# Performance work log

Hardware: AMD Instinct MI355X
Metric: run time of the kernel (lower is better)

The kernel has to match this reference:

```python
import jax, jax.numpy as jnp
import numpy as np

BASE = 7.0  # ModularPhaseNorm modulus


def _plane_rotate(x, theta):
    # Rotate the first 2*P dims of x in P independent 2D planes by learned angles theta [P].
    P = theta.shape[0]
    c, s = jnp.cos(theta), jnp.sin(theta)  # [P]
    head = x[..., : 2 * P].reshape(x.shape[:-1] + (P, 2))
    a, b = head[..., 0], head[..., 1]
    rot = jnp.stack([c * a - s * b, s * a + c * b], axis=-1)
    rot = rot.reshape(x.shape[:-1] + (2 * P,))
    return jnp.concatenate([rot, x[..., 2 * P :]], axis=-1)


def _modular_phase_norm(x, gamma, beta, base=BASE):
    # Wrap activations into [-base/2, base/2) (modular phase), then affine per-channel.
    wrapped = x - base * jnp.floor(x / base + 0.5)
    return gamma * wrapped + beta


def setup_inputs() -> dict:
    key = jax.random.key(0)
    ks = jax.random.split(key, 8)
    B, F, T, H = 8192, 4096, 9, 32
    team_paths = jax.random.normal(ks[0], (B, F, T), dtype=jnp.float32)
    W1 = jax.random.normal(ks[1], (F, H), dtype=jnp.float32) / np.sqrt(F)
    b1 = jnp.zeros((H,), dtype=jnp.float32)
    theta1 = jax.random.normal(ks[2], (2,), dtype=jnp.float32)  # num_rotation_planes=2
    gamma = jnp.ones((H,), dtype=jnp.float32)
    beta = jnp.zeros((H,), dtype=jnp.float32)
    W2 = jax.random.normal(ks[3], (H, 1), dtype=jnp.float32) / np.sqrt(H)
    b2 = jnp.zeros((1,), dtype=jnp.float32)
    theta2 = jax.random.normal(ks[4], (2,), dtype=jnp.float32)
    return {"team_paths": team_paths, "theta1": theta1, "W1": W1, "b1": b1,
            "gamma": gamma, "beta": beta, "theta2": theta2, "W2": W2, "b2": b2}


def reference(team_paths, theta1, W1, b1, gamma, beta, theta2, W2, b2):
    # Batch the per-member Python loop: [B, F, T] -> [B, T, F]
    x = jnp.transpose(team_paths, (0, 2, 1))
    # eidosTransform(feature_dim -> 32, 2 rotation planes)
    h = _plane_rotate(x, theta1)
    h = jnp.einsum("btf,fh->bth", h, W1) + b1
    # ModularPhaseNorm(32, base=7)
    h = _modular_phase_norm(h, gamma, beta)
    # eidosTransform(32 -> 1, 2 rotation planes)
    h = _plane_rotate(h, theta2)
    scores = jnp.einsum("bth,ho->bto", h, W2)[..., 0] + b2[0]  # [B, T]
    return jax.nn.softmax(scores, axis=1)
```

## Files before the change

kernel.cpp:

```cpp
#include <hip/hip_runtime.h>
#include <math.h>

typedef float f2v __attribute__((ext_vector_type(2)));
typedef float f4v __attribute__((ext_vector_type(4)));

#define NTILE 16
#define TILE_W 2304
#define FT 36864

__global__ __launch_bounds__(256) void scorer_kernel(
    const float* __restrict__ x,
    const float* __restrict__ th1,
    const float* __restrict__ W1,
    const float* __restrict__ b1,
    const float* __restrict__ gamma,
    const float* __restrict__ beta,
    const float* __restrict__ th2,
    const float* __restrict__ W2,
    const float* __restrict__ b2p,
    float* __restrict__ out)
{
    __shared__ __align__(16) float xl[2 * TILE_W];
    const int tid = threadIdx.x;
    const int hg  = tid & 7;
    const int fc  = tid >> 3;
    const int wv  = tid >> 6;
    const float* xb = x + (size_t)blockIdx.x * FT;

    f2v acc[9][2];
    #pragma unroll
    for (int t = 0; t < 9; ++t) {
        acc[t][0] = (f2v){0.f, 0.f};
        acc[t][1] = (f2v){0.f, 0.f};
    }

    int laddr[9];
    #pragma unroll
    for (int j = 0; j < 9; ++j) {
        int w = (j < 4) ? tid * 4 + j
              : (j < 8) ? 1024 + tid * 4 + (j - 4)
                        : 2048 + tid;
        int f = (unsigned)w / 9u;
        int t = w - 9 * f;
        laddr[j] = t * 256 + f;
    }

    f4v s04 = __builtin_nontemporal_load((const f4v*)(xb + tid * 4));
    f4v s47 = __builtin_nontemporal_load((const f4v*)(xb + 1024 + tid * 4));
    float s8 = __builtin_nontemporal_load(xb + 2048 + tid);

    const f4v* __restrict__ W1v = (const f4v*)W1;
    int cur = 0;
    for (int tile = 0; tile < NTILE; ++tile) {
        __syncthreads();
        float* lb = &xl[cur * TILE_W];
        lb[laddr[0]] = s04.x; lb[laddr[1]] = s04.y;
        lb[laddr[2]] = s04.z; lb[laddr[3]] = s04.w;
        lb[laddr[4]] = s47.x; lb[laddr[5]] = s47.y;
        lb[laddr[6]] = s47.z; lb[laddr[7]] = s47.w;
        lb[laddr[8]] = s8;
        __syncthreads();
        if (tile + 1 < NTILE) {
            const float* gt = xb + (size_t)(tile + 1) * TILE_W;
            s04 = __builtin_nontemporal_load((const f4v*)(gt + tid * 4));
            s47 = __builtin_nontemporal_load((const f4v*)(gt + 1024 + tid * 4));
            s8  = __builtin_nontemporal_load(gt + 2048 + tid);
        }
        if (tile == 0) {
            if (tid < 18) {
                int p = tid / 9, t = tid - p * 9;
                float c = cosf(th1[p]), sn = sinf(th1[p]);
                float a  = xl[t * 256 + 2 * p];
                float bv = xl[t * 256 + 2 * p + 1];
                xl[t * 256 + 2 * p]     = c * a - sn * bv;
                xl[t * 256 + 2 * p + 1] = sn * a + c * bv;
            }
            __syncthreads();
        }
        const int fb = tile * 256;
        f2v wlo[8], whi[8];
        #pragma unroll
        for (int i = 0; i < 8; ++i) {
            f4v wq = W1v[(size_t)(fb + fc * 8 + i) * 8 + hg];
            wlo[i] = (f2v){wq.x, wq.y};
            whi[i] = (f2v){wq.z, wq.w};
        }
        const float* xr = &xl[cur * TILE_W + fc * 8];
        #pragma unroll
        for (int t = 0; t < 9; ++t) {
            f4v xa = *(const f4v*)(xr + t * 256);
            f4v xc = *(const f4v*)(xr + t * 256 + 4);
            acc[t][0] += (f2v){xa.x, xa.x} * wlo[0]; acc[t][1] += (f2v){xa.x, xa.x} * whi[0];
            acc[t][0] += (f2v){xa.y, xa.y} * wlo[1]; acc[t][1] += (f2v){xa.y, xa.y} * whi[1];
            acc[t][0] += (f2v){xa.z, xa.z} * wlo[2]; acc[t][1] += (f2v){xa.z, xa.z} * whi[2];
            acc[t][0] += (f2v){xa.w, xa.w} * wlo[3]; acc[t][1] += (f2v){xa.w, xa.w} * whi[3];
            acc[t][0] += (f2v){xc.x, xc.x} * wlo[4]; acc[t][1] += (f2v){xc.x, xc.x} * whi[4];
            acc[t][0] += (f2v){xc.y, xc.y} * wlo[5]; acc[t][1] += (f2v){xc.y, xc.y} * whi[5];
            acc[t][0] += (f2v){xc.z, xc.z} * wlo[6]; acc[t][1] += (f2v){xc.z, xc.z} * whi[6];
            acc[t][0] += (f2v){xc.w, xc.w} * wlo[7]; acc[t][1] += (f2v){xc.w, xc.w} * whi[7];
        }
        cur ^= 1;
    }

    const int lane = tid & 63;
    float* red = xl;
    float* redbase = &red[(wv * 8 + lane) * 36];
    #pragma unroll
    for (int t = 0; t < 9; ++t)
        #pragma unroll
        for (int jv = 0; jv < 2; ++jv) {
            f2v v = acc[t][jv];
            v.x += __shfl_xor(v.x, 8);  v.y += __shfl_xor(v.y, 8);
            v.x += __shfl_xor(v.x, 16); v.y += __shfl_xor(v.y, 16);
            v.x += __shfl_xor(v.x, 32); v.y += __shfl_xor(v.y, 32);
            if (lane < 8) {
                redbase[t * 4 + jv * 2]     = v.x;
                redbase[t * 4 + jv * 2 + 1] = v.y;
            }
        }
    __syncthreads();

    for (int o = tid; o < 288; o += 256) {
        int h = o & 31, t = o >> 5;
        int hg2 = h >> 2, j = h & 3;
        int idx = t * 4 + j;
        float v = red[(0 * 8 + hg2) * 36 + idx]
                + red[(1 * 8 + hg2) * 36 + idx]
                + red[(2 * 8 + hg2) * 36 + idx]
                + red[(3 * 8 + hg2) * 36 + idx];
        v += b1[h];
        float wr = v - 7.0f * floorf(v / 7.0f + 0.5f);
        xl[1200 + o] = gamma[h] * wr + beta[h];
    }
    __syncthreads();

    if (tid < 9) {
        const float* g = &xl[1200 + tid * 32];
        float c0 = cosf(th2[0]), s0 = sinf(th2[0]);
        float c1 = cosf(th2[1]), s1 = sinf(th2[1]);
        float sc = (c0 * g[0] - s0 * g[1]) * W2[0]
                 + (s0 * g[0] + c0 * g[1]) * W2[1]
                 + (c1 * g[2] - s1 * g[3]) * W2[2]
                 + (s1 * g[2] + c1 * g[3]) * W2[3];
        #pragma unroll
        for (int h = 4; h < 32; ++h) sc += g[h] * W2[h];
        sc += b2p[0];
        xl[1500 + tid] = sc;
    }
    __syncthreads();

    if (tid < 9) {
        const float* sb = &xl[1500];
        float m = sb[0];
        #pragma unroll
        for (int k = 1; k < 9; ++k) m = fmaxf(m, sb[k]);
        float den = 0.f;
        #pragma unroll
        for (int k = 0; k < 9; ++k) den += expf(sb[k] - m);
        out[(size_t)blockIdx.x * 9 + tid] = expf(sb[tid] - m) / den;
    }
}

extern "C" void kernel_launch(void* const* d_in, const int* in_sizes, int n_in,
                              void* d_out, int out_size, void* d_ws, size_t ws_size,
                              hipStream_t stream) {
    const float* x     = (const float*)d_in[0];
    const float* th1   = (const float*)d_in[1];
    const float* W1    = (const float*)d_in[2];
    const float* b1    = (const float*)d_in[3];
    const float* gamma = (const float*)d_in[4];
    const float* beta  = (const float*)d_in[5];
    const float* th2   = (const float*)d_in[6];
    const float* W2    = (const float*)d_in[7];
    const float* b2    = (const float*)d_in[8];
    float* out = (float*)d_out;

    const int B = in_sizes[0] / FT;
    dim3 grid(B), block(256);
    hipLaunchKernelGGL(scorer_kernel, grid, block, 0, stream,
                       x, th1, W1, b1, gamma, beta, th2, W2, b2, out);
}
```

Measured before the change: 426.0 us.

## Remap threads to 4 features x 8 hidden units and pad LDS rows

Reassigns each thread from 8 features x 4 hidden outputs to 4 features x 8 hidden outputs, doubling accumulators per thread and halving W1 rows read per thread. LDS rows are padded from 256 to 260 floats to reduce bank conflicts on the per-timestep reads. The cross-lane reduction gains one shuffle stage and the reduction and scratch layouts are reworked to match. Register pressure rises from the larger accumulator array.

```diff
diff --git a/kernel.cpp b/kernel.cpp
--- a/kernel.cpp
+++ b/kernel.cpp
@@ -5,7 +5,8 @@
 typedef float f4v __attribute__((ext_vector_type(4)));
 
 #define NTILE 16
-#define TILE_W 2304
+#define FPAD 260
+#define TILE_PAD (9 * FPAD)
 #define FT 36864
 
 __global__ __launch_bounds__(256) void scorer_kernel(
@@ -20,19 +21,18 @@
     const float* __restrict__ b2p,
     float* __restrict__ out)
 {
-    __shared__ __align__(16) float xl[2 * TILE_W];
+    __shared__ __align__(16) float xl[2 * TILE_PAD];
     const int tid = threadIdx.x;
-    const int hg  = tid & 7;
-    const int fc  = tid >> 3;
+    const int hg  = tid & 3;
+    const int fc  = tid >> 2;
     const int wv  = tid >> 6;
     const float* xb = x + (size_t)blockIdx.x * FT;
 
-    f2v acc[9][2];
+    f2v acc[9][4];
     #pragma unroll
-    for (int t = 0; t < 9; ++t) {
-        acc[t][0] = (f2v){0.f, 0.f};
-        acc[t][1] = (f2v){0.f, 0.f};
-    }
+    for (int t = 0; t < 9; ++t)
+        #pragma unroll
+        for (int q = 0; q < 4; ++q) acc[t][q] = (f2v){0.f, 0.f};
 
     int laddr[9];
     #pragma unroll
@@ -42,7 +42,7 @@
                         : 2048 + tid;
         int f = (unsigned)w / 9u;
         int t = w - 9 * f;
-        laddr[j] = t * 256 + f;
+        laddr[j] = t * FPAD + f;
     }
 
     f4v s04 = __builtin_nontemporal_load((const f4v*)(xb + tid * 4));
@@ -53,7 +53,7 @@
     int cur = 0;
     for (int tile = 0; tile < NTILE; ++tile) {
         __syncthreads();
-        float* lb = &xl[cur * TILE_W];
+        float* lb = &xl[cur * TILE_PAD];
         lb[laddr[0]] = s04.x; lb[laddr[1]] = s04.y;
         lb[laddr[2]] = s04.z; lb[laddr[3]] = s04.w;
         lb[laddr[4]] = s47.x; lb[laddr[5]] = s47.y;
@@ -61,7 +61,7 @@
         lb[laddr[8]] = s8;
         __syncthreads();
         if (tile + 1 < NTILE) {
-            const float* gt = xb + (size_t)(tile + 1) * TILE_W;
+            const float* gt = xb + (size_t)(tile + 1) * 2304;
             s04 = __builtin_nontemporal_load((const f4v*)(gt + tid * 4));
             s47 = __builtin_nontemporal_load((const f4v*)(gt + 1024 + tid * 4));
             s8  = __builtin_nontemporal_load(gt + 2048 + tid);
@@ -70,72 +70,72 @@
             if (tid < 18) {
                 int p = tid / 9, t = tid - p * 9;
                 float c = cosf(th1[p]), sn = sinf(th1[p]);
-                float a  = xl[t * 256 + 2 * p];
-                float bv = xl[t * 256 + 2 * p + 1];
-                xl[t * 256 + 2 * p]     = c * a - sn * bv;
-                xl[t * 256 + 2 * p + 1] = sn * a + c * bv;
+                float a  = xl[t * FPAD + 2 * p];
+                float bv = xl[t * FPAD + 2 * p + 1];
+                xl[t * FPAD + 2 * p]     = c * a - sn * bv;
+                xl[t * FPAD + 2 * p + 1] = sn * a + c * bv;
             }
             __syncthreads();
         }
+        const float* xbuf = &xl[cur * TILE_PAD];
         const int fb = tile * 256;
-        f2v wlo[8], whi[8];
         #pragma unroll
-        for (int i = 0; i < 8; ++i) {
-            f4v wq = W1v[(size_t)(fb + fc * 8 + i) * 8 + hg];
-            wlo[i] = (f2v){wq.x, wq.y};
-            whi[i] = (f2v){wq.z, wq.w};
-        }
-        const float* xr = &xl[cur * TILE_W + fc * 8];
-        #pragma unroll
-        for (int t = 0; t < 9; ++t) {
-            f4v xa = *(const f4v*)(xr + t * 256);
-            f4v xc = *(const f4v*)(xr + t * 256 + 4);
-            acc[t][0] += (f2v){xa.x, xa.x} * wlo[0]; acc[t][1] += (f2v){xa.x, xa.x} * whi[0];
-            acc[t][0] += (f2v){xa.y, xa.y} * wlo[1]; acc[t][1] += (f2v){xa.y, xa.y} * whi[1];
-            acc[t][0] += (f2v){xa.z, xa.z} * wlo[2]; acc[t][1] += (f2v){xa.z, xa.z} * whi[2];
-            acc[t][0] += (f2v){xa.w, xa.w} * wlo[3]; acc[t][1] += (f2v){xa.w, xa.w} * whi[3];
-            acc[t][0] += (f2v){xc.x, xc.x} * wlo[4]; acc[t][1] += (f2v){xc.x, xc.x} * whi[4];
-            acc[t][0] += (f2v){xc.y, xc.y} * wlo[5]; acc[t][1] += (f2v){xc.y, xc.y} * whi[5];
-            acc[t][0] += (f2v){xc.z, xc.z} * wlo[6]; acc[t][1] += (f2v){xc.z, xc.z} * whi[6];
-            acc[t][0] += (f2v){xc.w, xc.w} * wlo[7]; acc[t][1] += (f2v){xc.w, xc.w} * whi[7];
+        for (int ih = 0; ih < 2; ++ih) {
+            const int f0 = fb + fc * 4 + ih * 2;
+            f4v wa0 = W1v[(size_t)f0 * 8 + hg * 2];
+            f4v wa1 = W1v[(size_t)f0 * 8 + hg * 2 + 1];
+            f4v wb0 = W1v[(size_t)(f0 + 1) * 8 + hg * 2];
+            f4v wb1 = W1v[(size_t)(f0 + 1) * 8 + hg * 2 + 1];
+            const float* xr = xbuf + fc * 4 + ih * 2;
+            #pragma unroll
+            for (int t = 0; t < 9; ++t) {
+                f2v xp = *(const f2v*)(xr + t * FPAD);
+                f2v xa = {xp.x, xp.x}, xc = {xp.y, xp.y};
+                acc[t][0] += xa * (f2v){wa0.x, wa0.y};
+                acc[t][1] += xa * (f2v){wa0.z, wa0.w};
+                acc[t][2] += xa * (f2v){wa1.x, wa1.y};
+                acc[t][3] += xa * (f2v){wa1.z, wa1.w};
+                acc[t][0] += xc * (f2v){wb0.x, wb0.y};
+                acc[t][1] += xc * (f2v){wb0.z, wb0.w};
+                acc[t][2] += xc * (f2v){wb1.x, wb1.y};
+                acc[t][3] += xc * (f2v){wb1.z, wb1.w};
+            }
         }
         cur ^= 1;
     }
 
     const int lane = tid & 63;
     float* red = xl;
-    float* redbase = &red[(wv * 8 + lane) * 36];
     #pragma unroll
     for (int t = 0; t < 9; ++t)
         #pragma unroll
-        for (int jv = 0; jv < 2; ++jv) {
-            f2v v = acc[t][jv];
+        for (int q = 0; q < 4; ++q) {
+            f2v v = acc[t][q];
+            v.x += __shfl_xor(v.x, 4);  v.y += __shfl_xor(v.y, 4);
             v.x += __shfl_xor(v.x, 8);  v.y += __shfl_xor(v.y, 8);
             v.x += __shfl_xor(v.x, 16); v.y += __shfl_xor(v.y, 16);
             v.x += __shfl_xor(v.x, 32); v.y += __shfl_xor(v.y, 32);
-            if (lane < 8) {
-                redbase[t * 4 + jv * 2]     = v.x;
-                redbase[t * 4 + jv * 2 + 1] = v.y;
-            }
+            if (lane < 4)
+                *(f2v*)&red[(wv * 4 + lane) * 72 + t * 8 + q * 2] = v;
         }
     __syncthreads();
 
     for (int o = tid; o < 288; o += 256) {
-        int h = o & 31, t = o >> 5;
-        int hg2 = h >> 2, j = h & 3;
-        int idx = t * 4 + j;
-        float v = red[(0 * 8 + hg2) * 36 + idx]
-                + red[(1 * 8 + hg2) * 36 + idx]
-                + red[(2 * 8 + hg2) * 36 + idx]
-                + red[(3 * 8 + hg2) * 36 + idx];
+        int t = o >> 5, h = o & 31;
+        int hg2 = h >> 3, hh = h & 7;
+        int idx = t * 8 + hh;
+        float v = red[(0 * 4 + hg2) * 72 + idx]
+                + red[(1 * 4 + hg2) * 72 + idx]
+                + red[(2 * 4 + hg2) * 72 + idx]
+                + red[(3 * 4 + hg2) * 72 + idx];
         v += b1[h];
         float wr = v - 7.0f * floorf(v / 7.0f + 0.5f);
-        xl[1200 + o] = gamma[h] * wr + beta[h];
+        xl[1152 + o] = gamma[h] * wr + beta[h];
     }
     __syncthreads();
 
     if (tid < 9) {
-        const float* g = &xl[1200 + tid * 32];
+        const float* g = &xl[1152 + tid * 32];
         float c0 = cosf(th2[0]), s0 = sinf(th2[0]);
         float c1 = cosf(th2[1]), s1 = sinf(th2[1]);
         float sc = (c0 * g[0] - s0 * g[1]) * W2[0]
@@ -145,12 +145,12 @@
         #pragma unroll
         for (int h = 4; h < 32; ++h) sc += g[h] * W2[h];
         sc += b2p[0];
-        xl[1500 + tid] = sc;
+        xl[1440 + tid] = sc;
     }
     __syncthreads();
 
     if (tid < 9) {
-        const float* sb = &xl[1500];
+        const float* sb = &xl[1440];
         float m = sb[0];
         #pragma unroll
         for (int k = 1; k < 9; ++k) m = fmaxf(m, sb[k]);
```

New measurement: 436.2 us. 2.4% more time.

## Assign one batch per wavefront and drop shared-memory staging and block syncs

Applied to the files above, without the earlier changes.

Each wavefront now handles one batch row: lanes load their contiguous x slices straight into registers, with no LDS transpose and no double-buffered tiles. The block size stays 256 and the grid shrinks by a factor of four. The second rotation is folded into W2, and the epilogue (bias, modular wrap, projection, softmax) runs with wave shuffles only, so all __syncthreads are gone. This removes LDS traffic and barrier stalls, but each lane now holds 18 float4 x values, which raises register pressure, and each wave streams W1 on its own.

```diff
diff --git a/kernel.cpp b/kernel.cpp
--- a/kernel.cpp
+++ b/kernel.cpp
@@ -4,9 +4,10 @@
 typedef float f2v __attribute__((ext_vector_type(2)));
 typedef float f4v __attribute__((ext_vector_type(4)));
 
-#define NTILE 16
-#define TILE_W 2304
 #define FT 36864
+#define NCHUNK 64
+
+#define XW(w) xv[(w) >> 2][(w) & 3]
 
 __global__ __launch_bounds__(256) void scorer_kernel(
     const float* __restrict__ x,
@@ -20,12 +21,18 @@
     const float* __restrict__ b2p,
     float* __restrict__ out)
 {
-    __shared__ __align__(16) float xl[2 * TILE_W];
-    const int tid = threadIdx.x;
-    const int hg  = tid & 7;
-    const int fc  = tid >> 3;
-    const int wv  = tid >> 6;
-    const float* xb = x + (size_t)blockIdx.x * FT;
+    const int tid  = threadIdx.x;
+    const int lane = tid & 63;
+    const int wv   = tid >> 6;
+    const int hg   = lane & 7;
+    const int fs   = lane >> 3;
+    const size_t batch = (size_t)blockIdx.x * 4 + wv;
+
+    const f4v* __restrict__ xv4 = (const f4v*)(x + batch * FT);
+    const f4v* __restrict__ w1v = (const f4v*)W1;
+
+    const float c0 = cosf(th1[0]), s0 = sinf(th1[0]);
+    const float c1 = cosf(th1[1]), s1 = sinf(th1[1]);
 
     f2v acc[9][2];
     #pragma unroll
@@ -34,130 +41,107 @@
         acc[t][1] = (f2v){0.f, 0.f};
     }
 
-    int laddr[9];
-    #pragma unroll
-    for (int j = 0; j < 9; ++j) {
-        int w = (j < 4) ? tid * 4 + j
-              : (j < 8) ? 1024 + tid * 4 + (j - 4)
-                        : 2048 + tid;
-        int f = (unsigned)w / 9u;
-        int t = w - 9 * f;
-        laddr[j] = t * 256 + f;
+    for (int c = 0; c < NCHUNK; ++c) {
+        f4v xv[18];
+        const int xbase = c * 144 + fs * 18;
+        #pragma unroll
+        for (int j = 0; j < 18; ++j)
+            xv[j] = __builtin_nontemporal_load(&xv4[xbase + j]);
+        f4v wr8[8];
+        const int frow = c * 64 + fs * 8;
+        #pragma unroll
+        for (int r = 0; r < 8; ++r)
+            wr8[r] = w1v[(size_t)(frow + r) * 8 + hg];
+
+        if (c == 0 && fs == 0) {
+            #pragma unroll
+            for (int t = 0; t < 9; ++t) {
+                float a = XW(t), b = XW(9 + t);
+                XW(t)     = c0 * a - s0 * b;
+                XW(9 + t) = s0 * a + c0 * b;
+                float a2 = XW(18 + t), b2 = XW(27 + t);
+                XW(18 + t) = c1 * a2 - s1 * b2;
+                XW(27 + t) = s1 * a2 + c1 * b2;
+            }
+        }
+
+        #pragma unroll
+        for (int r = 0; r < 8; ++r) {
+            f2v wlo = {wr8[r].x, wr8[r].y};
+            f2v whi = {wr8[r].z, wr8[r].w};
+            #pragma unroll
+            for (int t = 0; t < 9; ++t) {
+                const int w = r * 9 + t;
+                float xs = XW(w);
+                acc[t][0] += (f2v){xs, xs} * wlo;
+                acc[t][1] += (f2v){xs, xs} * whi;
+            }
+        }
     }
 
-    f4v s04 = __builtin_nontemporal_load((const f4v*)(xb + tid * 4));
-    f4v s47 = __builtin_nontemporal_load((const f4v*)(xb + 1024 + tid * 4));
-    float s8 = __builtin_nontemporal_load(xb + 2048 + tid);
-
-    const f4v* __restrict__ W1v = (const f4v*)W1;
-    int cur = 0;
-    for (int tile = 0; tile < NTILE; ++tile) {
-        __syncthreads();
-        float* lb = &xl[cur * TILE_W];
-        lb[laddr[0]] = s04.x; lb[laddr[1]] = s04.y;
-        lb[laddr[2]] = s04.z; lb[laddr[3]] = s04.w;
-        lb[laddr[4]] = s47.x; lb[laddr[5]] = s47.y;
-        lb[laddr[6]] = s47.z; lb[laddr[7]] = s47.w;
-        lb[laddr[8]] = s8;
-        __syncthreads();
-        if (tile + 1 < NTILE) {
-            const float* gt = xb + (size_t)(tile + 1) * TILE_W;
-            s04 = __builtin_nontemporal_load((const f4v*)(gt + tid * 4));
-            s47 = __builtin_nontemporal_load((const f4v*)(gt + 1024 + tid * 4));
-            s8  = __builtin_nontemporal_load(gt + 2048 + tid);
-        }
-        if (tile == 0) {
-            if (tid < 18) {
-                int p = tid / 9, t = tid - p * 9;
-                float c = cosf(th1[p]), sn = sinf(th1[p]);
-                float a  = xl[t * 256 + 2 * p];
-                float bv = xl[t * 256 + 2 * p + 1];
-                xl[t * 256 + 2 * p]     = c * a - sn * bv;
-                xl[t * 256 + 2 * p + 1] = sn * a + c * bv;
-            }
-            __syncthreads();
-        }
-        const int fb = tile * 256;
-        f2v wlo[8], whi[8];
-        #pragma unroll
-        for (int i = 0; i < 8; ++i) {
-            f4v wq = W1v[(size_t)(fb + fc * 8 + i) * 8 + hg];
-            wlo[i] = (f2v){wq.x, wq.y};
-            whi[i] = (f2v){wq.z, wq.w};
-        }
-        const float* xr = &xl[cur * TILE_W + fc * 8];
-        #pragma unroll
-        for (int t = 0; t < 9; ++t) {
-            f4v xa = *(const f4v*)(xr + t * 256);
-            f4v xc = *(const f4v*)(xr + t * 256 + 4);
-            acc[t][0] += (f2v){xa.x, xa.x} * wlo[0]; acc[t][1] += (f2v){xa.x, xa.x} * whi[0];
-            acc[t][0] += (f2v){xa.y, xa.y} * wlo[1]; acc[t][1] += (f2v){xa.y, xa.y} * whi[1];
-            acc[t][0] += (f2v){xa.z, xa.z} * wlo[2]; acc[t][1] += (f2v){xa.z, xa.z} * whi[2];
-            acc[t][0] += (f2v){xa.w, xa.w} * wlo[3]; acc[t][1] += (f2v){xa.w, xa.w} * whi[3];
-            acc[t][0] += (f2v){xc.x, xc.x} * wlo[4]; acc[t][1] += (f2v){xc.x, xc.x} * whi[4];
-            acc[t][0] += (f2v){xc.y, xc.y} * wlo[5]; acc[t][1] += (f2v){xc.y, xc.y} * whi[5];
-            acc[t][0] += (f2v){xc.z, xc.z} * wlo[6]; acc[t][1] += (f2v){xc.z, xc.z} * whi[6];
-            acc[t][0] += (f2v){xc.w, xc.w} * wlo[7]; acc[t][1] += (f2v){xc.w, xc.w} * whi[7];
-        }
-        cur ^= 1;
-    }
-
-    const int lane = tid & 63;
-    float* red = xl;
-    float* redbase = &red[(wv * 8 + lane) * 36];
     #pragma unroll
     for (int t = 0; t < 9; ++t)
         #pragma unroll
-        for (int jv = 0; jv < 2; ++jv) {
-            f2v v = acc[t][jv];
+        for (int p = 0; p < 2; ++p) {
+            f2v v = acc[t][p];
             v.x += __shfl_xor(v.x, 8);  v.y += __shfl_xor(v.y, 8);
             v.x += __shfl_xor(v.x, 16); v.y += __shfl_xor(v.y, 16);
             v.x += __shfl_xor(v.x, 32); v.y += __shfl_xor(v.y, 32);
-            if (lane < 8) {
-                redbase[t * 4 + jv * 2]     = v.x;
-                redbase[t * 4 + jv * 2 + 1] = v.y;
-            }
+            acc[t][p] = v;
         }
-    __syncthreads();
 
-    for (int o = tid; o < 288; o += 256) {
-        int h = o & 31, t = o >> 5;
-        int hg2 = h >> 2, j = h & 3;
-        int idx = t * 4 + j;
-        float v = red[(0 * 8 + hg2) * 36 + idx]
-                + red[(1 * 8 + hg2) * 36 + idx]
-                + red[(2 * 8 + hg2) * 36 + idx]
-                + red[(3 * 8 + hg2) * 36 + idx];
-        v += b1[h];
-        float wr = v - 7.0f * floorf(v / 7.0f + 0.5f);
-        xl[1200 + o] = gamma[h] * wr + beta[h];
+    const int h0 = hg * 4;
+    float b1q[4], gq[4], bq[4], w2q[4];
+    #pragma unroll
+    for (int j = 0; j < 4; ++j) {
+        b1q[j] = b1[h0 + j];
+        gq[j]  = gamma[h0 + j];
+        bq[j]  = beta[h0 + j];
+        w2q[j] = W2[h0 + j];
     }
-    __syncthreads();
+    if (hg == 0) {
+        const float c2 = cosf(th2[0]), s2 = sinf(th2[0]);
+        const float c3 = cosf(th2[1]), s3 = sinf(th2[1]);
+        float a = w2q[0], b = w2q[1];
+        w2q[0] =  c2 * a + s2 * b;
+        w2q[1] = -s2 * a + c2 * b;
+        float a2 = w2q[2], b2 = w2q[3];
+        w2q[2] =  c3 * a2 + s3 * b2;
+        w2q[3] = -s3 * a2 + c3 * b2;
+    }
 
-    if (tid < 9) {
-        const float* g = &xl[1200 + tid * 32];
-        float c0 = cosf(th2[0]), s0 = sinf(th2[0]);
-        float c1 = cosf(th2[1]), s1 = sinf(th2[1]);
-        float sc = (c0 * g[0] - s0 * g[1]) * W2[0]
-                 + (s0 * g[0] + c0 * g[1]) * W2[1]
-                 + (c1 * g[2] - s1 * g[3]) * W2[2]
-                 + (s1 * g[2] + c1 * g[3]) * W2[3];
+    float sc[9];
+    #pragma unroll
+    for (int t = 0; t < 9; ++t) {
+        float p = 0.f;
         #pragma unroll
-        for (int h = 4; h < 32; ++h) sc += g[h] * W2[h];
-        sc += b2p[0];
-        xl[1500 + tid] = sc;
+        for (int j = 0; j < 4; ++j) {
+            float v = acc[t][j >> 1][j & 1] + b1q[j];
+            float wr = v - 7.0f * floorf(v / 7.0f + 0.5f);
+            float g = gq[j] * wr + bq[j];
+            p += g * w2q[j];
+        }
+        sc[t] = p;
     }
-    __syncthreads();
 
-    if (tid < 9) {
-        const float* sb = &xl[1500];
-        float m = sb[0];
+    #pragma unroll
+    for (int t = 0; t < 9; ++t) {
+        sc[t] += __shfl_xor(sc[t], 1);
+        sc[t] += __shfl_xor(sc[t], 2);
+        sc[t] += __shfl_xor(sc[t], 4);
+        sc[t] += b2p[0];
+    }
+
+    float m = sc[0];
+    #pragma unroll
+    for (int t = 1; t < 9; ++t) m = fmaxf(m, sc[t]);
+    float e[9], den = 0.f;
+    #pragma unroll
+    for (int t = 0; t < 9; ++t) { e[t] = expf(sc[t] - m); den += e[t]; }
+    if (lane == 0) {
         #pragma unroll
-        for (int k = 1; k < 9; ++k) m = fmaxf(m, sb[k]);
-        float den = 0.f;
-        #pragma unroll
-        for (int k = 0; k < 9; ++k) den += expf(sb[k] - m);
-        out[(size_t)blockIdx.x * 9 + tid] = expf(sb[tid] - m) / den;
+        for (int t = 0; t < 9; ++t)
+            out[batch * 9 + t] = e[t] / den;
     }
 }
 
@@ -176,7 +160,7 @@
     float* out = (float*)d_out;
 
     const int B = in_sizes[0] / FT;
-    dim3 grid(B), block(256);
+    dim3 grid(B / 4), block(256);
     hipLaunchKernelGGL(scorer_kernel, grid, block, 0, stream,
                        x, th1, W1, b1, gamma, beta, th2, W2, b2, out);
 }
```

Result: slower. 825.1 us (+93.7%).
